# Performance work log

Hardware: AMD Instinct MI355X
Metric: run time of the kernel (lower is better)

The kernel has to match this reference:

```python
import jax, jax.numpy as jnp
import numpy as np

N_NODES = 20000
N_EDGES = 160000
N_GRAPHS = 100
IN_CH = 64
EDGE_DIM = 8
NEG_SLOPE = 0.2


def _gatv2(x, edge_index, edge_attr, Wl, Wr, We, att, b, heads, ch, n_nodes):
    # GATv2Conv: e_ij = att . leaky_relu(Wl x_j + Wr x_i [+ We e_ij]), softmax over dst i,
    # out_i = sum_j alpha_ij * (Wl x_j), concat heads, + bias.
    src, dst = edge_index[0], edge_index[1]
    xl = (x @ Wl).reshape(-1, heads, ch)  # [N,H,C] source-side transform
    xr = (x @ Wr).reshape(-1, heads, ch)  # [N,H,C] target-side transform
    m = xl[src] + xr[dst]                 # [E,H,C]
    if edge_attr is not None:
        m = m + (edge_attr @ We).reshape(-1, heads, ch)
    m = jax.nn.leaky_relu(m, NEG_SLOPE)
    logit = jnp.einsum('ehc,hc->eh', m, att)                     # [E,H]
    mx = jax.ops.segment_max(logit, dst, num_segments=n_nodes)   # [N,H]
    ex = jnp.exp(logit - mx[dst])
    den = jax.ops.segment_sum(ex, dst, num_segments=n_nodes)     # [N,H]
    alpha = ex / (den[dst] + 1e-16)                              # [E,H]
    out = jax.ops.segment_sum(alpha[:, :, None] * xl[src], dst, num_segments=n_nodes)
    return out.reshape(-1, heads * ch) + b


def setup_inputs() -> dict:
    key = jax.random.key(0)
    ks = jax.random.split(key, 24)
    def rn(k, shape, fan_in):
        return jax.random.normal(k, shape, dtype=jnp.float32) / np.sqrt(fan_in)
    inp = {}
    inp['x'] = jax.random.normal(ks[0], (N_NODES, IN_CH), dtype=jnp.float32)
    inp['edge_attr'] = jax.random.uniform(ks[1], (N_EDGES, EDGE_DIM), dtype=jnp.float32)
    inp['Wl1'] = rn(ks[2], (IN_CH, 1024), IN_CH)
    inp['Wr1'] = rn(ks[3], (IN_CH, 1024), IN_CH)
    inp['We1'] = rn(ks[4], (EDGE_DIM, 1024), EDGE_DIM)
    inp['att1'] = rn(ks[5], (4, 256), 256)
    inp['b1'] = jnp.zeros((1024,), jnp.float32)
    inp['Wl2'] = rn(ks[6], (1024, 256), 1024)
    inp['Wr2'] = rn(ks[7], (1024, 256), 1024)
    inp['We2'] = rn(ks[8], (EDGE_DIM, 256), EDGE_DIM)
    inp['att2'] = rn(ks[9], (4, 64), 64)
    inp['b2'] = jnp.zeros((256,), jnp.float32)
    inp['Wlp'] = rn(ks[10], (256, 384), 256)
    inp['Wrp'] = rn(ks[11], (256, 384), 256)
    inp['attp'] = rn(ks[12], (6, 64), 64)
    inp['bp'] = jnp.zeros((384,), jnp.float32)
    inp['Wfc1'] = rn(ks[13], (384, 64), 384)
    inp['bfc1'] = jnp.zeros((64,), jnp.float32)
    inp['Wfc2'] = rn(ks[14], (64, 1), 64)
    inp['bfc2'] = jnp.zeros((1,), jnp.float32)
    inp['edge_index'] = jax.random.randint(ks[15], (2, N_EDGES), 0, N_NODES, dtype=jnp.int32)
    inp['edge_index_master'] = jax.random.randint(ks[16], (2, N_EDGES), 0, N_NODES, dtype=jnp.int32)
    inp['n_nodes'] = jnp.full((N_GRAPHS,), N_NODES // N_GRAPHS, dtype=jnp.int32)
    return inp


def reference(x, edge_attr, Wl1, Wr1, We1, att1, b1, Wl2, Wr2, We2, att2, b2,
              Wlp, Wrp, attp, bp, Wfc1, bfc1, Wfc2, bfc2,
              edge_index, edge_index_master, n_nodes):
    h = _gatv2(x, edge_index, edge_attr, Wl1, Wr1, We1, att1, b1, 4, 256, N_NODES)
    h = jax.nn.relu(h)
    h = _gatv2(h, edge_index, edge_attr, Wl2, Wr2, We2, att2, b2, 4, 64, N_NODES)
    h = jax.nn.relu(h)
    h = _gatv2(h, edge_index_master, None, Wlp, Wrp, None, attp, bp, 6, 64, N_NODES)
    last_idx = jnp.cumsum(n_nodes) - 1          # master node = last node of each graph
    master = h[last_idx]                        # [G,384] (dropout p=0 -> identity)
    z = jax.nn.relu(master @ Wfc1 + bfc1)
    return z @ Wfc2 + bfc2                      # [G,1]
```

## Files before the change

### kernel.cpp

```cpp
#include <hip/hip_runtime.h>
#include <hip/hip_bf16.h>

#define DIV_UP(a,b) (((a)+(b)-1)/(b))

typedef __attribute__((ext_vector_type(8))) short short8;
typedef __attribute__((ext_vector_type(4))) float floatx4;

static __device__ __forceinline__ unsigned short f2bf(float v) {
    unsigned u = __builtin_bit_cast(unsigned, v);
    u += 0x7fffu + ((u >> 16) & 1u);
    return (unsigned short)(u >> 16);
}
static __device__ __forceinline__ float bflo(unsigned v) {
    return __builtin_bit_cast(float, v << 16);
}
static __device__ __forceinline__ float bfhi(unsigned v) {
    return __builtin_bit_cast(float, v & 0xffff0000u);
}

template <int CPL>
static __device__ __forceinline__ void load_bf16v(const unsigned short* p, float* d) {
    if constexpr (CPL == 8) {
        uint4 v = *(const uint4*)p;
        d[0] = bflo(v.x); d[1] = bfhi(v.x);
        d[2] = bflo(v.y); d[3] = bfhi(v.y);
        d[4] = bflo(v.z); d[5] = bfhi(v.z);
        d[6] = bflo(v.w); d[7] = bfhi(v.w);
    } else if constexpr (CPL == 4) {
        uint2 v = *(const uint2*)p;
        d[0] = bflo(v.x); d[1] = bfhi(v.x);
        d[2] = bflo(v.y); d[3] = bfhi(v.y);
    } else if constexpr (CPL == 2) {
        unsigned v = *(const unsigned*)p;
        d[0] = bflo(v); d[1] = bfhi(v);
    } else {
        d[0] = bflo(*p);
    }
}

template <int CPL>
static __device__ __forceinline__ void store_bf16v(unsigned short* p, const float* s) {
    unsigned short tmp[CPL];
#pragma unroll
    for (int c = 0; c < CPL; ++c) tmp[c] = f2bf(s[c]);
    if constexpr (CPL == 8) *(uint4*)p = *(uint4*)tmp;
    else if constexpr (CPL == 4) *(ushort4*)p = *(ushort4*)tmp;
    else if constexpr (CPL == 2) *(ushort2*)p = *(ushort2*)tmp;
    else p[0] = tmp[0];
}

static __device__ __forceinline__ void load_f32x8(const float* p, float* d) {
    float4 a = ((const float4*)p)[0];
    float4 b = ((const float4*)p)[1];
    d[0] = a.x; d[1] = a.y; d[2] = a.z; d[3] = a.w;
    d[4] = b.x; d[5] = b.y; d[6] = b.z; d[7] = b.w;
}

template <int CTRL>
static __device__ __forceinline__ float dpp_mv(float x) {
    int r = __builtin_amdgcn_update_dpp(0, __builtin_bit_cast(int, x), CTRL, 0xF, 0xF, false);
    return __builtin_bit_cast(float, r);
}
template <int G>
static __device__ __forceinline__ float group_reduce(float x) {
    x += dpp_mv<0xB1>(x);
    x += dpp_mv<0x4E>(x);
    x += dpp_mv<0x124>(x);
    x += dpp_mv<0x128>(x);
    if constexpr (G >= 32) x += __shfl_xor(x, 16, 64);
    if constexpr (G >= 64) x += __shfl_xor(x, 32, 64);
    return x;
}

__global__ void cvt_transpose2(const float* __restrict__ Wa, const float* __restrict__ Wb,
                               int K, int Nn, unsigned short* __restrict__ Wt) {
    int id = blockIdx.x * blockDim.x + threadIdx.x;
    int tot = K * Nn;
    if (id >= 2 * tot) return;
    const float* W = (id < tot) ? Wa : Wb;
    unsigned short* dst = Wt + ((id < tot) ? 0 : (size_t)Nn * K);
    int i = (id < tot) ? id : id - tot;
    int k = i % K, n = i / K;
    dst[(size_t)n * K + k] = f2bf(W[(size_t)k * Nn + n]);
}

__global__ void cvt_bf16(const float* __restrict__ in, unsigned short* __restrict__ out, int n) {
    int id = blockIdx.x * blockDim.x + threadIdx.x;
    if (id < n) out[id] = f2bf(in[id]);
}

__global__ __launch_bounds__(256) void gemm_mfma(
    const unsigned short* __restrict__ A, const unsigned short* __restrict__ Bt,
    unsigned short* __restrict__ C, int M, int Ntot, int K) {
    constexpr int LDA = 40;
    __shared__ unsigned short As[128 * LDA];
    __shared__ unsigned short Bs[128 * LDA];
    const int tid = threadIdx.x;
    const int m0 = blockIdx.y * 128, n0 = blockIdx.x * 128;
    const int wave = tid >> 6, lane = tid & 63;
    const int wm = (wave >> 1) * 64, wn = (wave & 1) * 64;
    const int r15 = lane & 15, quad = lane >> 4;
    const int sr = tid >> 1, skc = tid & 1;
    floatx4 acc[4][4];
#pragma unroll
    for (int i = 0; i < 4; ++i)
#pragma unroll
        for (int j = 0; j < 4; ++j) acc[i][j] = (floatx4)0.f;

    for (int k0 = 0; k0 < K; k0 += 32) {
        uint4 a0 = make_uint4(0, 0, 0, 0), a1 = make_uint4(0, 0, 0, 0);
        int am = m0 + sr;
        if (am < M) {
            const unsigned short* ap = A + (size_t)am * K + k0 + skc * 16;
            a0 = *(const uint4*)ap;
            a1 = *(const uint4*)(ap + 8);
        }
        const unsigned short* bp = Bt + (size_t)(n0 + sr) * K + k0 + skc * 16;
        uint4 b0 = *(const uint4*)bp;
        uint4 b1 = *(const uint4*)(bp + 8);
        *(uint4*)(&As[sr * LDA + skc * 16]) = a0;
        *(uint4*)(&As[sr * LDA + skc * 16 + 8]) = a1;
        *(uint4*)(&Bs[sr * LDA + skc * 16]) = b0;
        *(uint4*)(&Bs[sr * LDA + skc * 16 + 8]) = b1;
        __syncthreads();
        short8 af[4], bfr[4];
#pragma unroll
        for (int i = 0; i < 4; ++i)
            af[i] = *(const short8*)(&As[(wm + i * 16 + r15) * LDA + quad * 8]);
#pragma unroll
        for (int j = 0; j < 4; ++j)
            bfr[j] = *(const short8*)(&Bs[(wn + j * 16 + r15) * LDA + quad * 8]);
#pragma unroll
        for (int i = 0; i < 4; ++i)
#pragma unroll
            for (int j = 0; j < 4; ++j)
                acc[i][j] = __builtin_amdgcn_mfma_f32_16x16x32_bf16(af[i], bfr[j], acc[i][j], 0, 0, 0);
        __syncthreads();
    }
#pragma unroll
    for (int i = 0; i < 4; ++i)
#pragma unroll
        for (int j = 0; j < 4; ++j)
#pragma unroll
            for (int r = 0; r < 4; ++r) {
                int m = m0 + wm + i * 16 + quad * 4 + r;
                int n = n0 + wn + j * 16 + r15;
                if (m < M) C[(size_t)m * Ntot + n] = f2bf(acc[i][j][r]);
            }
}

__global__ void count2_kernel(const int* __restrict__ dst0, const int* __restrict__ dst1,
                              int E, int N, int* __restrict__ cnt) {
    int e = blockIdx.x * blockDim.x + threadIdx.x;
    if (e < E) atomicAdd(&cnt[dst0[e]], 1);
    else if (e < 2 * E) atomicAdd(&cnt[N + dst1[e - E]], 1);
}

__global__ __launch_bounds__(1024) void scan_kernel(const int* __restrict__ cnt_all, int N,
                                                    int* __restrict__ off_all, int* __restrict__ cur_all) {
    const int* cnt = cnt_all + blockIdx.x * N;
    int* off = off_all + blockIdx.x * (N + 1);
    int* cur = cur_all + blockIdx.x * N;
    __shared__ int part[1024];
    int t = threadIdx.x;
    int per = (N + 1023) >> 10;
    int base = t * per;
    int s = 0;
    for (int i = 0; i < per; ++i) { int idx = base + i; if (idx < N) s += cnt[idx]; }
    part[t] = s;
    __syncthreads();
    for (int d2 = 1; d2 < 1024; d2 <<= 1) {
        int v = (t >= d2) ? part[t - d2] : 0;
        __syncthreads();
        part[t] += v;
        __syncthreads();
    }
    int pre = (t == 0) ? 0 : part[t - 1];
    for (int i = 0; i < per; ++i) {
        int idx = base + i;
        if (idx < N) { off[idx] = pre; cur[idx] = pre; pre += cnt[idx]; }
    }
    if (t == 1023) off[N] = part[1023];
}

__global__ void fill2_kernel(const int* __restrict__ src0, const int* __restrict__ dst0,
                             const int* __restrict__ src1, const int* __restrict__ dst1,
                             int E, int N, int* __restrict__ cur, int2* __restrict__ edges) {
    int e = blockIdx.x * blockDim.x + threadIdx.x;
    if (e < E) {
        int p = atomicAdd(&cur[dst0[e]], 1);
        edges[p] = make_int2(src0[e], e);
    } else if (e < 2 * E) {
        int i = e - E;
        int p = atomicAdd(&cur[N + dst1[i]], 1);
        edges[E + p] = make_int2(src1[i], i);
    }
}

template <int D, int C, int CB, int WPN, bool RELU>
__global__ __launch_bounds__(256) void attn_hase(
    const unsigned short* __restrict__ xlr, const float* __restrict__ ea,
    const float* __restrict__ We, const float* __restrict__ att,
    const int2* __restrict__ edges, const int* __restrict__ off,
    const float* __restrict__ bias, unsigned short* __restrict__ outp, int N) {
    constexpr int CPL = CB / 64;
    constexpr int HW = CB / C;
    constexpr int G = 64 / HW;
    constexpr int NPB = 4 / WPN;
    constexpr int QP = CB * 4 / CPL;
    __shared__ float wsh[8 * D];
    for (int f4 = threadIdx.x; f4 < 2 * D; f4 += 256) {
        int k = f4 / (D / 4);
        int c = (f4 - k * (D / 4)) * 4;
        int b = c / CB, cc = c - b * CB;
        int ln = cc / CPL, q = (cc % CPL) / 4;
        int dst = k * (D / 4) + (b * CB + q * QP + ln * 4) / 4;
        ((float4*)wsh)[dst] = ((const float4*)We)[f4];
    }
    __syncthreads();

    const int wid = threadIdx.x >> 6, lane = threadIdx.x & 63;
    const int wv = wid % WPN, wn = wid / WPN;
    const int c0 = wv * CB + lane * CPL;
    const float* wb = wsh + wv * CB + lane * 4;

    float att_r[CPL], bias_r[CPL];
#pragma unroll
    for (int c = 0; c < CPL; ++c) { att_r[c] = att[c0 + c]; bias_r[c] = bias[c0 + c]; }

    for (int node = blockIdx.x * NPB + wn; node < N; node += gridDim.x * NPB) {
        float xr_r[CPL];
        load_bf16v<CPL>(xlr + (size_t)node * (2 * D) + D + c0, xr_r);
        float m = -1e30f, l = 0.f, acc[CPL];
#pragma unroll
        for (int c = 0; c < CPL; ++c) acc[c] = 0.f;

        const int jb = off[node], je = off[node + 1];
        int j = jb;
        for (; j + 2 <= je; j += 2) {
            int2 e0 = edges[j], e1 = edges[j + 1];
            float ev0[8], ev1[8];
            load_f32x8(ea + (size_t)e0.y * 8, ev0);
            load_f32x8(ea + (size_t)e1.y * 8, ev1);
            float xv0[CPL], xv1[CPL];
            load_bf16v<CPL>(xlr + (size_t)e0.x * (2 * D) + c0, xv0);
            load_bf16v<CPL>(xlr + (size_t)e1.x * (2 * D) + c0, xv1);
            float z0[CPL], z1[CPL];
#pragma unroll
            for (int c = 0; c < CPL; ++c) {
                z0[c] = xv0[c] + xr_r[c];
                z1[c] = xv1[c] + xr_r[c];
            }
#pragma unroll
            for (int k = 0; k < 8; ++k) {
#pragma unroll
                for (int q = 0; q < CPL / 4; ++q) {
                    float4 w4 = *(const float4*)(wb + k * D + q * QP);
                    z0[q * 4 + 0] = fmaf(ev0[k], w4.x, z0[q * 4 + 0]);
                    z0[q * 4 + 1] = fmaf(ev0[k], w4.y, z0[q * 4 + 1]);
                    z0[q * 4 + 2] = fmaf(ev0[k], w4.z, z0[q * 4 + 2]);
                    z0[q * 4 + 3] = fmaf(ev0[k], w4.w, z0[q * 4 + 3]);
                    z1[q * 4 + 0] = fmaf(ev1[k], w4.x, z1[q * 4 + 0]);
                    z1[q * 4 + 1] = fmaf(ev1[k], w4.y, z1[q * 4 + 1]);
                    z1[q * 4 + 2] = fmaf(ev1[k], w4.z, z1[q * 4 + 2]);
                    z1[q * 4 + 3] = fmaf(ev1[k], w4.w, z1[q * 4 + 3]);
                }
            }
            float lg0 = 0.f, lg1 = 0.f;
#pragma unroll
            for (int c = 0; c < CPL; ++c) {
                float a0 = z0[c] > 0.f ? z0[c] : 0.2f * z0[c];
                float a1 = z1[c] > 0.f ? z1[c] : 0.2f * z1[c];
                lg0 = fmaf(att_r[c], a0, lg0);
                lg1 = fmaf(att_r[c], a1, lg1);
            }
            lg0 = group_reduce<G>(lg0);
            lg1 = group_reduce<G>(lg1);
            float mn = fmaxf(m, fmaxf(lg0, lg1));
            float sc = __expf(m - mn);
            float p0 = __expf(lg0 - mn);
            float p1 = __expf(lg1 - mn);
            m = mn;
            l = fmaf(l, sc, p0 + p1);
#pragma unroll
            for (int c = 0; c < CPL; ++c)
                acc[c] = fmaf(acc[c], sc, fmaf(p0, xv0[c], p1 * xv1[c]));
        }
        if (j < je) {
            int2 e0 = edges[j];
            float ev0[8], xv0[CPL];
            load_f32x8(ea + (size_t)e0.y * 8, ev0);
            load_bf16v<CPL>(xlr + (size_t)e0.x * (2 * D) + c0, xv0);
            float z0[CPL];
#pragma unroll
            for (int c = 0; c < CPL; ++c) z0[c] = xv0[c] + xr_r[c];
#pragma unroll
            for (int k = 0; k < 8; ++k) {
#pragma unroll
                for (int q = 0; q < CPL / 4; ++q) {
                    float4 w4 = *(const float4*)(wb + k * D + q * QP);
                    z0[q * 4 + 0] = fmaf(ev0[k], w4.x, z0[q * 4 + 0]);
                    z0[q * 4 + 1] = fmaf(ev0[k], w4.y, z0[q * 4 + 1]);
                    z0[q * 4 + 2] = fmaf(ev0[k], w4.z, z0[q * 4 + 2]);
                    z0[q * 4 + 3] = fmaf(ev0[k], w4.w, z0[q * 4 + 3]);
                }
            }
            float lg0 = 0.f;
#pragma unroll
            for (int c = 0; c < CPL; ++c) {
                float a0 = z0[c] > 0.f ? z0[c] : 0.2f * z0[c];
                lg0 = fmaf(att_r[c], a0, lg0);
            }
            lg0 = group_reduce<G>(lg0);
            float mn = fmaxf(m, lg0);
            float sc = __expf(m - mn);
            float p0 = __expf(lg0 - mn);
            m = mn;
            l = fmaf(l, sc, p0);
#pragma unroll
            for (int c = 0; c < CPL; ++c) acc[c] = fmaf(acc[c], sc, p0 * xv0[c]);
        }

        float inv = 1.f / (l + 1e-16f);
        float r[CPL];
#pragma unroll
        for (int c = 0; c < CPL; ++c) {
            r[c] = fmaf(acc[c], inv, bias_r[c]);
            if constexpr (RELU) r[c] = fmaxf(r[c], 0.f);
        }
        store_bf16v<CPL>(outp + (size_t)node * D + c0, r);
    }
}

template <int D, int C, int CB, bool RELU>
static __device__ __forceinline__ void attn_wave3(
    const unsigned short* __restrict__ xlr, const float* __restrict__ att,
    const int2* __restrict__ edges, int jb, int je,
    const float* __restrict__ bias, float* __restrict__ outp,
    int node, int cb, int lane) {
    constexpr int CPL = CB / 64;
    constexpr int HW = CB / C;
    constexpr int G = 64 / HW;
    const int c0 = cb + lane * CPL;

    float xr_r[CPL], att_r[CPL];
    load_bf16v<CPL>(xlr + (size_t)node * (2 * D) + D + c0, xr_r);
#pragma unroll
    for (int c = 0; c < CPL; ++c) att_r[c] = att[c0 + c];

    float m = -1e30f, l = 0.f, acc[CPL];
#pragma unroll
    for (int c = 0; c < CPL; ++c) acc[c] = 0.f;

    int j = jb;
    for (; j + 2 <= je; j += 2) {
        int2 e0 = edges[j], e1 = edges[j + 1];
        float xv0[CPL], xv1[CPL];
        load_bf16v<CPL>(xlr + (size_t)e0.x * (2 * D) + c0, xv0);
        load_bf16v<CPL>(xlr + (size_t)e1.x * (2 * D) + c0, xv1);
        float lg0 = 0.f, lg1 = 0.f;
#pragma unroll
        for (int c = 0; c < CPL; ++c) {
            float z0 = xv0[c] + xr_r[c];
            float z1 = xv1[c] + xr_r[c];
            z0 = z0 > 0.f ? z0 : 0.2f * z0;
            z1 = z1 > 0.f ? z1 : 0.2f * z1;
            lg0 = fmaf(att_r[c], z0, lg0);
            lg1 = fmaf(att_r[c], z1, lg1);
        }
        lg0 = group_reduce<G>(lg0);
        lg1 = group_reduce<G>(lg1);
        float mn = fmaxf(m, fmaxf(lg0, lg1));
        float sc = __expf(m - mn);
        float p0 = __expf(lg0 - mn);
        float p1 = __expf(lg1 - mn);
        m = mn;
        l = fmaf(l, sc, p0 + p1);
#pragma unroll
        for (int c = 0; c < CPL; ++c)
            acc[c] = fmaf(acc[c], sc, fmaf(p0, xv0[c], p1 * xv1[c]));
    }
    if (j < je) {
        int2 e0 = edges[j];
        float xv0[CPL];
        load_bf16v<CPL>(xlr + (size_t)e0.x * (2 * D) + c0, xv0);
        float lg0 = 0.f;
#pragma unroll
        for (int c = 0; c < CPL; ++c) {
            float z = xv0[c] + xr_r[c];
            z = z > 0.f ? z : 0.2f * z;
            lg0 = fmaf(att_r[c], z, lg0);
        }
        lg0 = group_reduce<G>(lg0);
        float mn = fmaxf(m, lg0);
        float sc = __expf(m - mn);
        float p0 = __expf(lg0 - mn);
        m = mn;
        l = fmaf(l, sc, p0);
#pragma unroll
        for (int c = 0; c < CPL; ++c) acc[c] = fmaf(acc[c], sc, p0 * xv0[c]);
    }

    float inv = 1.f / (l + 1e-16f);
    float* out = outp + (size_t)node * D + c0;
    float tmp[CPL];
#pragma unroll
    for (int c = 0; c < CPL; ++c) {
        float r = fmaf(acc[c], inv, bias[c0 + c]);
        if constexpr (RELU) r = fmaxf(r, 0.f);
        tmp[c] = r;
    }
    if constexpr (CPL == 4) *(float4*)out = *(float4*)tmp;
    else if constexpr (CPL == 2) *(float2*)out = *(float2*)tmp;
    else out[0] = tmp[0];
}

template <int D, int C, int CB0, int CB1, bool RELU>
__global__ __launch_bounds__(256) void attn_noe(
    const unsigned short* __restrict__ xlr, const float* __restrict__ att,
    const int2* __restrict__ edges, const int* __restrict__ off,
    const float* __restrict__ bias, float* __restrict__ outp, int N) {
    const int wid = threadIdx.x >> 6, lane = threadIdx.x & 63;
    const int gw = blockIdx.x * 4 + wid;
    const int node = gw >> 1, wv = gw & 1;
    if (node >= N) return;
    const int jb = off[node], je = off[node + 1];
    if (wv == 0)
        attn_wave3<D, C, CB0, RELU>(xlr, att, edges, jb, je, bias, outp, node, 0, lane);
    else
        attn_wave3<D, C, CB1, RELU>(xlr, att, edges, jb, je, bias, outp, node, CB0, lane);
}

__global__ void mlp_kernel(const float* __restrict__ h3, const int* __restrict__ nn,
                           const float* __restrict__ Wfc1, const float* __restrict__ bfc1,
                           const float* __restrict__ Wfc2, const float* __restrict__ bfc2,
                           float* __restrict__ out, int G) {
    int g = blockIdx.x, t = threadIdx.x;
    int s = 0;
    for (int k = 0; k <= g; ++k) s += nn[k];
    const float* row = h3 + (size_t)(s - 1) * 384;
    float z = bfc1[t];
    for (int k = 0; k < 384; ++k) z = fmaf(row[k], Wfc1[k * 64 + t], z);
    z = fmaxf(z, 0.f);
    float v = z * Wfc2[t];
#pragma unroll
    for (int o = 32; o; o >>= 1) v += __shfl_xor(v, o, 64);
    if (t == 0) out[g] = v + bfc2[0];
}

extern "C" void kernel_launch(void* const* d_in, const int* in_sizes, int n_in,
                              void* d_out, int out_size, void* d_ws, size_t ws_size,
                              hipStream_t stream) {
    const float* x    = (const float*)d_in[0];
    const float* ea   = (const float*)d_in[1];
    const float* Wl1  = (const float*)d_in[2];
    const float* Wr1  = (const float*)d_in[3];
    const float* We1  = (const float*)d_in[4];
    const float* att1 = (const float*)d_in[5];
    const float* b1   = (const float*)d_in[6];
    const float* Wl2  = (const float*)d_in[7];
    const float* Wr2  = (const float*)d_in[8];
    const float* We2  = (const float*)d_in[9];
    const float* att2 = (const float*)d_in[10];
    const float* b2   = (const float*)d_in[11];
    const float* Wlp  = (const float*)d_in[12];
    const float* Wrp  = (const float*)d_in[13];
    const float* attp = (const float*)d_in[14];
    const float* bp   = (const float*)d_in[15];
    const float* Wfc1 = (const float*)d_in[16];
    const float* bfc1 = (const float*)d_in[17];
    const float* Wfc2 = (const float*)d_in[18];
    const float* bfc2 = (const float*)d_in[19];
    const int* ei     = (const int*)d_in[20];
    const int* eim    = (const int*)d_in[21];
    const int* nn     = (const int*)d_in[22];

    const int N = in_sizes[0] / 64;
    const int E = in_sizes[20] / 2;
    const int G = in_sizes[22];
    const int* src1 = ei,  *dst1 = ei + E;
    const int* srcm = eim, *dstm = eim + E;

    char* w = (char*)d_ws;
    size_t o = 0;
    auto alloc = [&](size_t b) { size_t r = o; o += (b + 255) & ~(size_t)255; return r; };
    char* R1 = w + alloc((size_t)N * 2048 * 2);
    unsigned short* xlr1 = (unsigned short*)R1;
    unsigned short* xlr3 = (unsigned short*)R1;
    float* h3 = (float*)(R1 + (size_t)N * 768 * 2 + 256);
    unsigned short* h1   = (unsigned short*)(w + alloc((size_t)N * 1024 * 2));
    unsigned short* xlr2 = (unsigned short*)(w + alloc((size_t)N * 512 * 2));
    unsigned short* h2   = (unsigned short*)(w + alloc((size_t)N * 256 * 2));
    unsigned short* xbf  = (unsigned short*)(w + alloc((size_t)N * 64 * 2));
    unsigned short* wt1  = (unsigned short*)(w + alloc((size_t)2048 * 64 * 2));
    unsigned short* wt2  = (unsigned short*)(w + alloc((size_t)512 * 1024 * 2));
    unsigned short* wt3  = (unsigned short*)(w + alloc((size_t)768 * 256 * 2));
    int*  cnt   = (int*)(w + alloc((size_t)2 * N * 4));
    int*  off   = (int*)(w + alloc((size_t)2 * (N + 1) * 4));
    int*  cur   = (int*)(w + alloc((size_t)2 * N * 4));
    int2* edges = (int2*)(w + alloc((size_t)2 * E * 8 + 4096));
    (void)ws_size; (void)n_in; (void)out_size;

    dim3 blk(256);

    cvt_transpose2<<<DIV_UP(2 * 64 * 1024, 256), blk, 0, stream>>>(Wl1, Wr1, 64, 1024, wt1);
    cvt_transpose2<<<DIV_UP(2 * 1024 * 256, 256), blk, 0, stream>>>(Wl2, Wr2, 1024, 256, wt2);
    cvt_transpose2<<<DIV_UP(2 * 256 * 384, 256), blk, 0, stream>>>(Wlp, Wrp, 256, 384, wt3);
    cvt_bf16<<<DIV_UP(N * 64, 256), blk, 0, stream>>>(x, xbf, N * 64);

    hipMemsetAsync(cnt, 0, (size_t)2 * N * 4, stream);
    count2_kernel<<<DIV_UP(2 * E, 256), blk, 0, stream>>>(dst1, dstm, E, N, cnt);
    scan_kernel<<<2, 1024, 0, stream>>>(cnt, N, off, cur);
    fill2_kernel<<<DIV_UP(2 * E, 256), blk, 0, stream>>>(src1, dst1, srcm, dstm, E, N, cur, edges);
    const int* off3 = off + (N + 1);
    int2* edges3 = edges + E;

    gemm_mfma<<<dim3(2048 / 128, DIV_UP(N, 128)), blk, 0, stream>>>(xbf, wt1, xlr1, N, 2048, 64);
    attn_hase<1024, 256, 512, 2, true><<<2560, blk, 0, stream>>>(
        xlr1, ea, We1, att1, edges, off, b1, h1, N);

    gemm_mfma<<<dim3(512 / 128, DIV_UP(N, 128)), blk, 0, stream>>>(h1, wt2, xlr2, N, 512, 1024);
    attn_hase<256, 64, 256, 1, true><<<1280, blk, 0, stream>>>(
        xlr2, ea, We2, att2, edges, off, b2, h2, N);

    gemm_mfma<<<dim3(768 / 128, DIV_UP(N, 128)), blk, 0, stream>>>(h2, wt3, xlr3, N, 768, 256);
    attn_noe<384, 64, 256, 128, false><<<DIV_UP(N, 2), blk, 0, stream>>>(
        xlr3, attp, edges3, off3, bp, h3, N);

    mlp_kernel<<<G, 64, 0, stream>>>(h3, nn, Wfc1, bfc1, Wfc2, bfc2, (float*)d_out, G);
}
```

Before: 497.7 us.

## Unroll edge loops by four, fuse prep kernels, scalarize CSR offsets

Each attention kernel now processes edges four at a time through a templated group helper. This raises memory-level parallelism on the gathered rows and amortizes the online-softmax rescale over more edges. The four weight-transpose and cast launches are merged into one prep kernel to cut launch overhead. CSR offsets are also made wave-uniform via readfirstlane, and bias is read at the end instead of held in registers. The wider unroll raises register pressure, which may lower occupancy in the large-CPL layer-1 kernel.

```diff
diff --git a/kernel.cpp b/kernel.cpp
--- a/kernel.cpp
+++ b/kernel.cpp
@@ -49,13 +49,6 @@
     else p[0] = tmp[0];
 }
 
-static __device__ __forceinline__ void load_f32x8(const float* p, float* d) {
-    float4 a = ((const float4*)p)[0];
-    float4 b = ((const float4*)p)[1];
-    d[0] = a.x; d[1] = a.y; d[2] = a.z; d[3] = a.w;
-    d[4] = b.x; d[5] = b.y; d[6] = b.z; d[7] = b.w;
-}
-
 template <int CTRL>
 static __device__ __forceinline__ float dpp_mv(float x) {
     int r = __builtin_amdgcn_update_dpp(0, __builtin_bit_cast(int, x), CTRL, 0xF, 0xF, false);
@@ -72,21 +65,32 @@
     return x;
 }
 
-__global__ void cvt_transpose2(const float* __restrict__ Wa, const float* __restrict__ Wb,
-                               int K, int Nn, unsigned short* __restrict__ Wt) {
+static __device__ __forceinline__ void tr_pair(const float* Wa, const float* Wb, int K, int Nn,
+                                               unsigned short* Wt, int i) {
+    int tot = K * Nn;
+    const float* W = (i < tot) ? Wa : Wb;
+    unsigned short* dst = Wt + ((i < tot) ? 0 : (size_t)Nn * K);
+    int ii = (i < tot) ? i : i - tot;
+    int k = ii % K, n = ii / K;
+    dst[(size_t)n * K + k] = f2bf(W[(size_t)k * Nn + n]);
+}
+
+__global__ void prep_all(const float* __restrict__ x,
+                         const float* __restrict__ Wl1, const float* __restrict__ Wr1,
+                         const float* __restrict__ Wl2, const float* __restrict__ Wr2,
+                         const float* __restrict__ Wlp, const float* __restrict__ Wrp,
+                         unsigned short* __restrict__ xbf,
+                         unsigned short* __restrict__ wt1, unsigned short* __restrict__ wt2,
+                         unsigned short* __restrict__ wt3, int N) {
+    const int S1 = 2 * 64 * 1024, S2 = 2 * 1024 * 256, S3 = 2 * 256 * 384;
     int id = blockIdx.x * blockDim.x + threadIdx.x;
-    int tot = K * Nn;
-    if (id >= 2 * tot) return;
-    const float* W = (id < tot) ? Wa : Wb;
-    unsigned short* dst = Wt + ((id < tot) ? 0 : (size_t)Nn * K);
-    int i = (id < tot) ? id : id - tot;
-    int k = i % K, n = i / K;
-    dst[(size_t)n * K + k] = f2bf(W[(size_t)k * Nn + n]);
-}
-
-__global__ void cvt_bf16(const float* __restrict__ in, unsigned short* __restrict__ out, int n) {
-    int id = blockIdx.x * blockDim.x + threadIdx.x;
-    if (id < n) out[id] = f2bf(in[id]);
+    if (id < S1) tr_pair(Wl1, Wr1, 64, 1024, wt1, id);
+    else if (id < S1 + S2) tr_pair(Wl2, Wr2, 1024, 256, wt2, id - S1);
+    else if (id < S1 + S2 + S3) tr_pair(Wlp, Wrp, 256, 384, wt3, id - S1 - S2);
+    else {
+        int i = id - S1 - S2 - S3;
+        if (i < N * 64) xbf[i] = f2bf(x[i]);
+    }
 }
 
 __global__ __launch_bounds__(256) void gemm_mfma(
@@ -194,6 +198,73 @@
         int i = e - E;
         int p = atomicAdd(&cur[N + dst1[i]], 1);
         edges[E + p] = make_int2(src1[i], i);
+    }
+}
+
+template <int D, int CPL, int QP, int G, int NE>
+static __device__ __forceinline__ void hase_group(
+    const unsigned short* __restrict__ xlr, const float* __restrict__ ea,
+    const float* wb, const float (&att_r)[CPL], const float (&xr_r)[CPL],
+    const int2* ep , int c0,
+    float& m, float& l, float (&acc)[CPL]) {
+    int2 e[NE];
+#pragma unroll
+    for (int n = 0; n < NE; ++n) e[n] = ep[n];
+    float ev[NE][8];
+#pragma unroll
+    for (int n = 0; n < NE; ++n) {
+        float4 a = ((const float4*)(ea + (size_t)e[n].y * 8))[0];
+        float4 b = ((const float4*)(ea + (size_t)e[n].y * 8))[1];
+        ev[n][0] = a.x; ev[n][1] = a.y; ev[n][2] = a.z; ev[n][3] = a.w;
+        ev[n][4] = b.x; ev[n][5] = b.y; ev[n][6] = b.z; ev[n][7] = b.w;
+    }
+    float xv[NE][CPL], z[NE][CPL];
+#pragma unroll
+    for (int n = 0; n < NE; ++n) {
+        load_bf16v<CPL>(xlr + (size_t)e[n].x * (2 * D) + c0, xv[n]);
+#pragma unroll
+        for (int c = 0; c < CPL; ++c) z[n][c] = xv[n][c] + xr_r[c];
+    }
+#pragma unroll
+    for (int k = 0; k < 8; ++k) {
+#pragma unroll
+        for (int q = 0; q < CPL / 4; ++q) {
+            float4 w4 = *(const float4*)(wb + k * D + q * QP);
+#pragma unroll
+            for (int n = 0; n < NE; ++n) {
+                z[n][q * 4 + 0] = fmaf(ev[n][k], w4.x, z[n][q * 4 + 0]);
+                z[n][q * 4 + 1] = fmaf(ev[n][k], w4.y, z[n][q * 4 + 1]);
+                z[n][q * 4 + 2] = fmaf(ev[n][k], w4.z, z[n][q * 4 + 2]);
+                z[n][q * 4 + 3] = fmaf(ev[n][k], w4.w, z[n][q * 4 + 3]);
+            }
+        }
+    }
+    float lg[NE];
+#pragma unroll
+    for (int n = 0; n < NE; ++n) {
+        lg[n] = 0.f;
+#pragma unroll
+        for (int c = 0; c < CPL; ++c) {
+            float a = z[n][c] > 0.f ? z[n][c] : 0.2f * z[n][c];
+            lg[n] = fmaf(att_r[c], a, lg[n]);
+        }
+        lg[n] = group_reduce<G>(lg[n]);
+    }
+    float mn = m;
+#pragma unroll
+    for (int n = 0; n < NE; ++n) mn = fmaxf(mn, lg[n]);
+    float sc = __expf(m - mn);
+    float p[NE], ps = 0.f;
+#pragma unroll
+    for (int n = 0; n < NE; ++n) { p[n] = __expf(lg[n] - mn); ps += p[n]; }
+    m = mn;
+    l = fmaf(l, sc, ps);
+#pragma unroll
+    for (int c = 0; c < CPL; ++c) {
+        float t = p[0] * xv[0][c];
+#pragma unroll
+        for (int n = 1; n < NE; ++n) t = fmaf(p[n], xv[n][c], t);
+        acc[c] = fmaf(acc[c], sc, t);
     }
 }
 
@@ -224,9 +295,9 @@
     const int c0 = wv * CB + lane * CPL;
     const float* wb = wsh + wv * CB + lane * 4;
 
-    float att_r[CPL], bias_r[CPL];
-#pragma unroll
-    for (int c = 0; c < CPL; ++c) { att_r[c] = att[c0 + c]; bias_r[c] = bias[c0 + c]; }
+    float att_r[CPL];
+#pragma unroll
+    for (int c = 0; c < CPL; ++c) att_r[c] = att[c0 + c];
 
     for (int node = blockIdx.x * NPB + wn; node < N; node += gridDim.x * NPB) {
         float xr_r[CPL];
@@ -235,100 +306,64 @@
 #pragma unroll
         for (int c = 0; c < CPL; ++c) acc[c] = 0.f;
 
-        const int jb = off[node], je = off[node + 1];
+        const int jb = __builtin_amdgcn_readfirstlane(off[node]);
+        const int je = __builtin_amdgcn_readfirstlane(off[node + 1]);
         int j = jb;
-        for (; j + 2 <= je; j += 2) {
-            int2 e0 = edges[j], e1 = edges[j + 1];
-            float ev0[8], ev1[8];
-            load_f32x8(ea + (size_t)e0.y * 8, ev0);
-            load_f32x8(ea + (size_t)e1.y * 8, ev1);
-            float xv0[CPL], xv1[CPL];
-            load_bf16v<CPL>(xlr + (size_t)e0.x * (2 * D) + c0, xv0);
-            load_bf16v<CPL>(xlr + (size_t)e1.x * (2 * D) + c0, xv1);
-            float z0[CPL], z1[CPL];
-#pragma unroll
-            for (int c = 0; c < CPL; ++c) {
-                z0[c] = xv0[c] + xr_r[c];
-                z1[c] = xv1[c] + xr_r[c];
-            }
-#pragma unroll
-            for (int k = 0; k < 8; ++k) {
-#pragma unroll
-                for (int q = 0; q < CPL / 4; ++q) {
-                    float4 w4 = *(const float4*)(wb + k * D + q * QP);
-                    z0[q * 4 + 0] = fmaf(ev0[k], w4.x, z0[q * 4 + 0]);
-                    z0[q * 4 + 1] = fmaf(ev0[k], w4.y, z0[q * 4 + 1]);
-                    z0[q * 4 + 2] = fmaf(ev0[k], w4.z, z0[q * 4 + 2]);
-                    z0[q * 4 + 3] = fmaf(ev0[k], w4.w, z0[q * 4 + 3]);
-                    z1[q * 4 + 0] = fmaf(ev1[k], w4.x, z1[q * 4 + 0]);
-                    z1[q * 4 + 1] = fmaf(ev1[k], w4.y, z1[q * 4 + 1]);
-                    z1[q * 4 + 2] = fmaf(ev1[k], w4.z, z1[q * 4 + 2]);
-                    z1[q * 4 + 3] = fmaf(ev1[k], w4.w, z1[q * 4 + 3]);
-                }
-            }
-            float lg0 = 0.f, lg1 = 0.f;
-#pragma unroll
-            for (int c = 0; c < CPL; ++c) {
-                float a0 = z0[c] > 0.f ? z0[c] : 0.2f * z0[c];
-                float a1 = z1[c] > 0.f ? z1[c] : 0.2f * z1[c];
-                lg0 = fmaf(att_r[c], a0, lg0);
-                lg1 = fmaf(att_r[c], a1, lg1);
-            }
-            lg0 = group_reduce<G>(lg0);
-            lg1 = group_reduce<G>(lg1);
-            float mn = fmaxf(m, fmaxf(lg0, lg1));
-            float sc = __expf(m - mn);
-            float p0 = __expf(lg0 - mn);
-            float p1 = __expf(lg1 - mn);
-            m = mn;
-            l = fmaf(l, sc, p0 + p1);
-#pragma unroll
-            for (int c = 0; c < CPL; ++c)
-                acc[c] = fmaf(acc[c], sc, fmaf(p0, xv0[c], p1 * xv1[c]));
-        }
-        if (j < je) {
-            int2 e0 = edges[j];
-            float ev0[8], xv0[CPL];
-            load_f32x8(ea + (size_t)e0.y * 8, ev0);
-            load_bf16v<CPL>(xlr + (size_t)e0.x * (2 * D) + c0, xv0);
-            float z0[CPL];
-#pragma unroll
-            for (int c = 0; c < CPL; ++c) z0[c] = xv0[c] + xr_r[c];
-#pragma unroll
-            for (int k = 0; k < 8; ++k) {
-#pragma unroll
-                for (int q = 0; q < CPL / 4; ++q) {
-                    float4 w4 = *(const float4*)(wb + k * D + q * QP);
-                    z0[q * 4 + 0] = fmaf(ev0[k], w4.x, z0[q * 4 + 0]);
-                    z0[q * 4 + 1] = fmaf(ev0[k], w4.y, z0[q * 4 + 1]);
-                    z0[q * 4 + 2] = fmaf(ev0[k], w4.z, z0[q * 4 + 2]);
-                    z0[q * 4 + 3] = fmaf(ev0[k], w4.w, z0[q * 4 + 3]);
-                }
-            }
-            float lg0 = 0.f;
-#pragma unroll
-            for (int c = 0; c < CPL; ++c) {
-                float a0 = z0[c] > 0.f ? z0[c] : 0.2f * z0[c];
-                lg0 = fmaf(att_r[c], a0, lg0);
-            }
-            lg0 = group_reduce<G>(lg0);
-            float mn = fmaxf(m, lg0);
-            float sc = __expf(m - mn);
-            float p0 = __expf(lg0 - mn);
-            m = mn;
-            l = fmaf(l, sc, p0);
-#pragma unroll
-            for (int c = 0; c < CPL; ++c) acc[c] = fmaf(acc[c], sc, p0 * xv0[c]);
-        }
+        for (; j + 4 <= je; j += 4)
+            hase_group<D, CPL, QP, G, 4>(xlr, ea, wb, att_r, xr_r, edges + j, c0, m, l, acc);
+        for (; j < je; ++j)
+            hase_group<D, CPL, QP, G, 1>(xlr, ea, wb, att_r, xr_r, edges + j, c0, m, l, acc);
 
         float inv = 1.f / (l + 1e-16f);
         float r[CPL];
 #pragma unroll
         for (int c = 0; c < CPL; ++c) {
-            r[c] = fmaf(acc[c], inv, bias_r[c]);
+            r[c] = fmaf(acc[c], inv, bias[c0 + c]);
             if constexpr (RELU) r[c] = fmaxf(r[c], 0.f);
         }
         store_bf16v<CPL>(outp + (size_t)node * D + c0, r);
+    }
+}
+
+template <int D, int CPL, int G, int NE>
+static __device__ __forceinline__ void noe_group(
+    const unsigned short* __restrict__ xlr,
+    const float (&att_r)[CPL], const float (&xr_r)[CPL],
+    const int2* ep , int c0,
+    float& m, float& l, float (&acc)[CPL]) {
+    int2 e[NE];
+#pragma unroll
+    for (int n = 0; n < NE; ++n) e[n] = ep[n];
+    float xv[NE][CPL], lg[NE];
+#pragma unroll
+    for (int n = 0; n < NE; ++n)
+        load_bf16v<CPL>(xlr + (size_t)e[n].x * (2 * D) + c0, xv[n]);
+#pragma unroll
+    for (int n = 0; n < NE; ++n) {
+        lg[n] = 0.f;
+#pragma unroll
+        for (int c = 0; c < CPL; ++c) {
+            float z = xv[n][c] + xr_r[c];
+            z = z > 0.f ? z : 0.2f * z;
+            lg[n] = fmaf(att_r[c], z, lg[n]);
+        }
+        lg[n] = group_reduce<G>(lg[n]);
+    }
+    float mn = m;
+#pragma unroll
+    for (int n = 0; n < NE; ++n) mn = fmaxf(mn, lg[n]);
+    float sc = __expf(m - mn);
+    float p[NE], ps = 0.f;
+#pragma unroll
+    for (int n = 0; n < NE; ++n) { p[n] = __expf(lg[n] - mn); ps += p[n]; }
+    m = mn;
+    l = fmaf(l, sc, ps);
+#pragma unroll
+    for (int c = 0; c < CPL; ++c) {
+        float t = p[0] * xv[0][c];
+#pragma unroll
+        for (int n = 1; n < NE; ++n) t = fmaf(p[n], xv[n][c], t);
+        acc[c] = fmaf(acc[c], sc, t);
     }
 }
 
@@ -353,53 +388,10 @@
     for (int c = 0; c < CPL; ++c) acc[c] = 0.f;
 
     int j = jb;
-    for (; j + 2 <= je; j += 2) {
-        int2 e0 = edges[j], e1 = edges[j + 1];
-        float xv0[CPL], xv1[CPL];
-        load_bf16v<CPL>(xlr + (size_t)e0.x * (2 * D) + c0, xv0);
-        load_bf16v<CPL>(xlr + (size_t)e1.x * (2 * D) + c0, xv1);
-        float lg0 = 0.f, lg1 = 0.f;
-#pragma unroll
-        for (int c = 0; c < CPL; ++c) {
-            float z0 = xv0[c] + xr_r[c];
-            float z1 = xv1[c] + xr_r[c];
-            z0 = z0 > 0.f ? z0 : 0.2f * z0;
-            z1 = z1 > 0.f ? z1 : 0.2f * z1;
-            lg0 = fmaf(att_r[c], z0, lg0);
-            lg1 = fmaf(att_r[c], z1, lg1);
-        }
-        lg0 = group_reduce<G>(lg0);
-        lg1 = group_reduce<G>(lg1);
-        float mn = fmaxf(m, fmaxf(lg0, lg1));
-        float sc = __expf(m - mn);
-        float p0 = __expf(lg0 - mn);
-        float p1 = __expf(lg1 - mn);
-        m = mn;
-        l = fmaf(l, sc, p0 + p1);
-#pragma unroll
-        for (int c = 0; c < CPL; ++c)
-            acc[c] = fmaf(acc[c], sc, fmaf(p0, xv0[c], p1 * xv1[c]));
-    }
-    if (j < je) {
-        int2 e0 = edges[j];
-        float xv0[CPL];
-        load_bf16v<CPL>(xlr + (size_t)e0.x * (2 * D) + c0, xv0);
-        float lg0 = 0.f;
-#pragma unroll
-        for (int c = 0; c < CPL; ++c) {
-            float z = xv0[c] + xr_r[c];
-            z = z > 0.f ? z : 0.2f * z;
-            lg0 = fmaf(att_r[c], z, lg0);
-        }
-        lg0 = group_reduce<G>(lg0);
-        float mn = fmaxf(m, lg0);
-        float sc = __expf(m - mn);
-        float p0 = __expf(lg0 - mn);
-        m = mn;
-        l = fmaf(l, sc, p0);
-#pragma unroll
-        for (int c = 0; c < CPL; ++c) acc[c] = fmaf(acc[c], sc, p0 * xv0[c]);
-    }
+    for (; j + 4 <= je; j += 4)
+        noe_group<D, CPL, G, 4>(xlr, att_r, xr_r, edges + j, c0, m, l, acc);
+    for (; j < je; ++j)
+        noe_group<D, CPL, G, 1>(xlr, att_r, xr_r, edges + j, c0, m, l, acc);
 
     float inv = 1.f / (l + 1e-16f);
     float* out = outp + (size_t)node * D + c0;
@@ -424,7 +416,8 @@
     const int gw = blockIdx.x * 4 + wid;
     const int node = gw >> 1, wv = gw & 1;
     if (node >= N) return;
-    const int jb = off[node], je = off[node + 1];
+    const int jb = __builtin_amdgcn_readfirstlane(off[node]);
+    const int je = __builtin_amdgcn_readfirstlane(off[node + 1]);
     if (wv == 0)
         attn_wave3<D, C, CB0, RELU>(xlr, att, edges, jb, je, bias, outp, node, 0, lane);
     else
@@ -503,10 +496,11 @@
 
     dim3 blk(256);
 
-    cvt_transpose2<<<DIV_UP(2 * 64 * 1024, 256), blk, 0, stream>>>(Wl1, Wr1, 64, 1024, wt1);
-    cvt_transpose2<<<DIV_UP(2 * 1024 * 256, 256), blk, 0, stream>>>(Wl2, Wr2, 1024, 256, wt2);
-    cvt_transpose2<<<DIV_UP(2 * 256 * 384, 256), blk, 0, stream>>>(Wlp, Wrp, 256, 384, wt3);
-    cvt_bf16<<<DIV_UP(N * 64, 256), blk, 0, stream>>>(x, xbf, N * 64);
+    {
+        int tot = 2 * 64 * 1024 + 2 * 1024 * 256 + 2 * 256 * 384 + N * 64;
+        prep_all<<<DIV_UP(tot, 256), blk, 0, stream>>>(x, Wl1, Wr1, Wl2, Wr2, Wlp, Wrp,
+                                                       xbf, wt1, wt2, wt3, N);
+    }
 
     hipMemsetAsync(cnt, 0, (size_t)2 * N * 4, stream);
     count2_kernel<<<DIV_UP(2 * E, 256), blk, 0, stream>>>(dst1, dstm, E, N, cnt);
```

Result: faster. 423.5 us (-14.9%).
